# Optimization experiments

Hardware: AMD Instinct MI355X
Metric: run time of the kernel (lower is better)

## Reference

```python
import jax, jax.numpy as jnp
import numpy as np
import math

N, C_IN, H, W = 8, 256, 64, 64
C_ATT, C_OUT = 128, 256
BN_EPS = 1e-5


def conv_bn_relu(x, w, gamma, beta, mean, var):
    # 1x1 conv (no bias) + BatchNorm (eval mode) + ReLU
    y = jnp.einsum('oc,nchw->nohw', w, x)
    inv = gamma / jnp.sqrt(var + BN_EPS)
    y = y * inv[None, :, None, None] + (beta - mean * inv)[None, :, None, None]
    return jax.nn.relu(y)


def setup_inputs() -> dict:
    key = jax.random.key(0)
    ks = jax.random.split(key, 12)
    x = jax.random.normal(ks[0], (N, C_IN, H, W), dtype=jnp.float32)
    mask = jnp.ones((N, 1, H, W), dtype=jnp.float32)
    reduc_w = jax.random.normal(ks[1], (C_OUT, C_IN), dtype=jnp.float32) * (1.0 / math.sqrt(C_IN))
    reduc_gamma = jnp.ones((C_OUT,), dtype=jnp.float32)
    reduc_beta = jnp.zeros((C_OUT,), dtype=jnp.float32)
    reduc_mean = jax.random.normal(ks[2], (C_OUT,), dtype=jnp.float32) * 0.1
    reduc_var = jax.random.uniform(ks[3], (C_OUT,), dtype=jnp.float32) + 0.5
    att_w = jax.random.normal(ks[4], (C_ATT, C_IN), dtype=jnp.float32) * (1.0 / math.sqrt(C_IN))
    att_gamma = jnp.ones((C_ATT,), dtype=jnp.float32)
    att_beta = jnp.zeros((C_ATT,), dtype=jnp.float32)
    att_mean = jax.random.normal(ks[5], (C_ATT,), dtype=jnp.float32) * 0.1
    att_var = jax.random.uniform(ks[6], (C_ATT,), dtype=jnp.float32) + 0.5
    return {
        'x': x, 'mask': mask,
        'reduc_w': reduc_w, 'reduc_gamma': reduc_gamma, 'reduc_beta': reduc_beta,
        'reduc_mean': reduc_mean, 'reduc_var': reduc_var,
        'att_w': att_w, 'att_gamma': att_gamma, 'att_beta': att_beta,
        'att_mean': att_mean, 'att_var': att_var,
    }


def reference(x, mask, reduc_w, reduc_gamma, reduc_beta, reduc_mean, reduc_var,
              att_w, att_gamma, att_beta, att_mean, att_var):
    n, _, h, w = x.shape
    x_feat = conv_bn_relu(x, reduc_w, reduc_gamma, reduc_beta, reduc_mean, reduc_var)   # [n,C_OUT,h,w]
    x_atten = conv_bn_relu(x, att_w, att_gamma, att_beta, att_mean, att_var)            # [n,C_ATT,h,w]
    c = x_atten.shape[1]
    q = x_atten.reshape(n, c, h * w)                                                    # [n,c,HW]
    # energy[n,i,j] = sum_c q[n,c,i]*q[n,c,j] / (1e-8 + sqrt(c))
    energy = jnp.einsum('nci,ncj->nij', q, q) / (1e-8 + math.sqrt(c))
    energy = energy + (mask.reshape(n, 1, h * w) - 1.0) * 1e8
    weight = jax.nn.softmax(energy, axis=2)                                             # [n,HW,HW]
    feat = x_feat.reshape(n, x_feat.shape[1], h * w)                                    # [n,C_OUT,HW]
    out = jnp.einsum('nij,ncj->nci', weight, feat)                                      # [n,C_OUT,HW]
    out = out.reshape(n, feat.shape[1], h, w)
    out = out * mask
    return out
```

## Files before the change

kernel.cpp:

```cpp
#include <hip/hip_runtime.h>
#include <cstdint>
#include <cstddef>

#define NB 8
#define CIN 256
#define HWX 4096
#define CF 256
#define CA 128
#define CT 384

typedef __attribute__((ext_vector_type(8))) _Float16 half8;
typedef __attribute__((ext_vector_type(8))) short short8;
typedef __attribute__((ext_vector_type(4))) short s16x4;
typedef __attribute__((ext_vector_type(4))) float f32x4;
typedef __attribute__((ext_vector_type(4))) unsigned int u32x4;
typedef __attribute__((ext_vector_type(2))) unsigned int u32x2;

#define OFF_WH   0
#define OFF_BIAS (CT*CIN*2)
#define OFF_FEAT (OFF_BIAS + CT*4)
#define OFF_Q    (OFF_FEAT + NB*CF*HWX*2)
#define OFF_NORM (OFF_Q + NB*HWX*CA*2)
#define OFF_G    (OFF_NORM + NB*HWX*4)

__device__ inline unsigned short f16_bits(float f) {
  _Float16 h = (_Float16)f;
  return __builtin_bit_cast(unsigned short, h);
}
__device__ inline half8 ld_half8(const unsigned short* p) {
  short8 r = *(const short8*)p;
  return __builtin_bit_cast(half8, r);
}

__device__ inline void g2l16(const void* g, void* l) {
  __builtin_amdgcn_global_load_lds(
      (const __attribute__((address_space(1))) unsigned int*)g,
      (__attribute__((address_space(3))) unsigned int*)l, 16, 0, 0);
}

__global__ __launch_bounds__(256) void fold_bn_k(
    const float* __restrict__ rw, const float* __restrict__ rg,
    const float* __restrict__ rb, const float* __restrict__ rm, const float* __restrict__ rv,
    const float* __restrict__ aw, const float* __restrict__ ag,
    const float* __restrict__ ab2, const float* __restrict__ am, const float* __restrict__ av,
    unsigned short* __restrict__ wh, float* __restrict__ bias, unsigned* __restrict__ Gmax) {
  int o = blockIdx.x, k = threadIdx.x;
  if (o == 0 && k < NB) Gmax[k] = 0u;
  const float* wsrc; float g, b, m, v;
  if (o < CF) { wsrc = rw + (size_t)o*CIN; g = rg[o]; b = rb[o]; m = rm[o]; v = rv[o]; }
  else { int oa = o - CF; wsrc = aw + (size_t)oa*CIN; g = ag[oa]; b = ab2[oa]; m = am[oa]; v = av[oa]; }
  float inv = g / sqrtf(v + 1e-5f);
  wh[(size_t)o*CIN + k] = f16_bits(wsrc[k] * inv);
  if (k == 0) bias[o] = b - m*inv;
}

__global__ __launch_bounds__(512, 4) void conv_k(
    const float* __restrict__ x, const unsigned short* __restrict__ wh,
    const float* __restrict__ bias, unsigned short* __restrict__ feat,
    unsigned short* __restrict__ q, float* __restrict__ normq,
    unsigned* __restrict__ Gmax) {
  __shared__ unsigned short sX[64*256];
  __shared__ float sGm[4];
  unsigned short (*sQr)[136] = (unsigned short(*)[136])sX;
  int b = blockIdx.x;
  int n = b & 7, pt0 = b >> 3;
  int p0 = pt0 * 64;
  int t = threadIdx.x;
  int w = t >> 6, lane = t & 63, quad = lane >> 4, col = lane & 15;
  const float* xn = x + (size_t)n*CIN*HWX;

  #pragma unroll
  for (int pass=0; pass<4; pass++) {
    int idx = pass*512 + t;
    int kp = idx >> 4, c4 = idx & 15;
    f32x4 a = *(const f32x4*)(xn + (size_t)(2*kp)*HWX + p0 + c4*4);
    f32x4 c = *(const f32x4*)(xn + (size_t)(2*kp+1)*HWX + p0 + c4*4);
    int unit = kp >> 2, off = kp & 3;
    #pragma unroll
    for (int j=0;j<4;j++) {
      int pos = c4*4 + j;
      unsigned dd = (unsigned)f16_bits(a[j]) | ((unsigned)f16_bits(c[j]) << 16);
      *(unsigned*)&sX[pos*256 + ((unit ^ (pos & 31)) << 3) + off*2] = dd;
    }
  }
  __syncthreads();

  f32x4 fzero = {0.f,0.f,0.f,0.f};
  f32x4 acc[4][3];
  #pragma unroll
  for (int pt=0;pt<4;pt++)
    #pragma unroll
    for (int ot=0;ot<3;ot++) acc[pt][ot] = fzero;

  int ocb = w*48;
  half8 B3[3];
  #pragma unroll
  for (int ot=0;ot<3;ot++)
    B3[ot] = ld_half8(wh + (size_t)(ocb + ot*16 + col)*CIN + quad*8);
  #pragma unroll
  for (int ks=0; ks<8; ks++) {
    half8 B3n[3];
    if (ks < 7) {
      #pragma unroll
      for (int ot=0;ot<3;ot++)
        B3n[ot] = ld_half8(wh + (size_t)(ocb + ot*16 + col)*CIN + (ks+1)*32 + quad*8);
    }
    half8 A4[4];
    #pragma unroll
    for (int pt=0;pt<4;pt++) {
      int pos = pt*16 + col;
      A4[pt] = ld_half8(&sX[pos*256 + (((ks*4 + quad) ^ (pos & 31)) << 3)]);
    }
    #pragma unroll
    for (int pt=0;pt<4;pt++)
      #pragma unroll
      for (int ot=0;ot<3;ot++)
        acc[pt][ot] = __builtin_amdgcn_mfma_f32_16x16x32_f16(A4[pt], B3[ot], acc[pt][ot], 0, 0, 0);
    if (ks < 7) {
      #pragma unroll
      for (int ot=0;ot<3;ot++) B3[ot] = B3n[ot];
    }
  }
  __syncthreads();

  float bv[3];
  #pragma unroll
  for (int ot=0;ot<3;ot++) bv[ot] = bias[ocb + ot*16 + col];
  #pragma unroll
  for (int pt=0;pt<4;pt++)
    #pragma unroll
    for (int ot=0;ot<3;ot++) {
      int oc = ocb + ot*16 + col;
      alignas(8) unsigned short u4[4];
      #pragma unroll
      for (int r=0;r<4;r++)
        u4[r] = f16_bits(fmaxf(acc[pt][ot][r] + bv[ot], 0.f));
      if (oc < CF) {
        *(u32x2*)(feat + (size_t)n*CF*HWX + (size_t)oc*HWX + p0 + pt*16 + quad*4) =
            *(const u32x2*)u4;
      } else {
        int cc = oc - CF;
        #pragma unroll
        for (int r=0;r<4;r++)
          sQr[pt*16 + quad*4 + r][cc] = u4[r];
      }
    }
  __syncthreads();

  if (t < 256) {
    int pos = t >> 2, seg = t & 3;
    const unsigned short* src = &sQr[pos][seg*32];
    unsigned short* dst = q + ((size_t)n*HWX + p0 + pos)*CA + seg*32;
    float s2 = 0.f;
    #pragma unroll
    for (int u=0;u<4;u++) {
      short8 v = *(const short8*)(src + u*8);
      *(short8*)(dst + u*8) = v;
      half8 h = __builtin_bit_cast(half8, v);
      #pragma unroll
      for (int e=0;e<8;e++) { float fe = (float)h[e]; s2 += fe*fe; }
    }
    s2 += __shfl_xor(s2, 1, 64);
    s2 += __shfl_xor(s2, 2, 64);
    if (seg == 0) normq[(size_t)n*HWX + p0 + pos] = sqrtf(s2);
    float mx = s2;
    mx = fmaxf(mx, __shfl_xor(mx, 4, 64));
    mx = fmaxf(mx, __shfl_xor(mx, 8, 64));
    mx = fmaxf(mx, __shfl_xor(mx, 16, 64));
    mx = fmaxf(mx, __shfl_xor(mx, 32, 64));
    if (lane == 0) sGm[t >> 6] = sqrtf(mx);
  }
  __syncthreads();
  if (t == 0) {
    float m01 = fmaxf(sGm[0], sGm[1]);
    float m23 = fmaxf(sGm[2], sGm[3]);
    atomicMax(Gmax + n, __float_as_uint(fmaxf(m01, m23)));
  }
}

__global__ __launch_bounds__(512, 4) void flash_k(
    const unsigned short* __restrict__ q, const unsigned short* __restrict__ feat,
    const float* __restrict__ mask, const float* __restrict__ normq,
    const unsigned* __restrict__ Gmax, float* __restrict__ out) {
  __shared__ alignas(16) unsigned short sQ0[64*128];
  __shared__ alignas(16) unsigned short sQ1[64*128];
  __shared__ alignas(16) unsigned short sP0[64][68];
  __shared__ alignas(16) unsigned short sP1[64][68];
  __shared__ float sM0[64];
  __shared__ float sM1[64];
  __shared__ float sL[2][64];
  int b = blockIdx.x;
  int n = b & 7, it = b >> 3;
  int i0 = it * 64;
  int t = threadIdx.x;
  int w = t >> 6, lane = t & 63, quad = lane >> 4, col = lane & 15;
  int wq = w & 3, wh = w >> 2;
  const unsigned short* q_n = q + (size_t)n*HWX*CA;
  const unsigned short* f_n = feat + (size_t)n*CF*HWX;
  const float* m_n = mask + (size_t)n*HWX;
  const int rloc = t >> 4 & 31, oct16 = t & 15;
  const float inv_s = 1.0f/(1e-8f + sqrtf(128.0f));

  auto stage_Q = [&](int j0, unsigned short* sQd, float* sMd) {
    #pragma unroll
    for (int c=0;c<2;c++) {
      int row = c*32 + rloc;
      int og = oct16 ^ (row & 15);
      g2l16(q_n + (size_t)(j0+row)*CA + og*8, &sQd[(size_t)row*128 + oct16*8]);
    }
    if (t < 16) g2l16(m_n + j0 + t*4, &sMd[t*4]);
  };

  half8 ah[4];
  {
    int arow = i0 + wq*16 + col;
    #pragma unroll
    for (int ks=0; ks<4; ks++)
      ah[ks] = ld_half8(q_n + (size_t)arow*CA + ks*32 + quad*8);
  }
  float Gn = __uint_as_float(Gmax[n]);
  float cvals[4];
  #pragma unroll
  for (int r=0;r<4;r++)
    cvals[r] = normq[(size_t)n*HWX + i0 + wq*16 + quad*4 + r] * Gn * inv_s - 5.0f;

  f32x4 fzero = {0.f,0.f,0.f,0.f};
  f32x4 o[4][2];
  #pragma unroll
  for (int ig=0;ig<4;ig++) { o[ig][0] = fzero; o[ig][1] = fzero; }
  float lrun[4] = {0.f,0.f,0.f,0.f};

  auto iter = [&](int ji, unsigned short* sQc, unsigned short (*sPc)[68], float* sMc,
                  unsigned short* sQn, float* sMn) {
    int j0 = ji*64;

    if (ji + 1 < 64) stage_Q(j0+64, sQn, sMn);

    half8 bF[2][2];
    #pragma unroll
    for (int ks2=0;ks2<2;ks2++)
      #pragma unroll
      for (int ct=0;ct<2;ct++) {
        int c = w*32 + ct*16 + col;
        bF[ks2][ct] = ld_half8(f_n + (size_t)c*HWX + j0 + ks2*32 + quad*8);
      }

    f32x4 s[2];
    s[0] = fzero; s[1] = fzero;
    __builtin_amdgcn_s_setprio(1);
    #pragma unroll
    for (int jt=0;jt<2;jt++) {
      int rowj = wh*32 + jt*16 + col;
      #pragma unroll
      for (int ks=0; ks<4; ks++) {
        int slot = (ks*4 + quad) ^ (rowj & 15);
        half8 bq = ld_half8(&sQc[rowj*128 + slot*8]);
        s[jt] = __builtin_amdgcn_mfma_f32_16x16x32_f16(ah[ks], bq, s[jt], 0, 0, 0);
      }
    }
    __builtin_amdgcn_s_setprio(0);

    #pragma unroll
    for (int jt=0;jt<2;jt++) {
      float mj = (sMc[wh*32 + jt*16 + col] - 1.f) * 1e8f;
      #pragma unroll
      for (int r=0;r<4;r++) {
        float pv = __expf(s[jt][r]*inv_s + mj - cvals[r]);
        lrun[r] += pv;
        sPc[wq*16 + quad*4 + r][wh*32 + jt*16 + col] = f16_bits(pv);
      }
    }

    __syncthreads();

    __builtin_amdgcn_s_setprio(1);
    #pragma unroll
    for (int ks2=0; ks2<2; ks2++) {
      half8 aP[4];
      #pragma unroll
      for (int ig=0;ig<4;ig++) {
        const unsigned short* pp = &sPc[ig*16 + col][ks2*32 + quad*8];
        s16x4 lo = *(const s16x4*)pp;
        s16x4 hi = *(const s16x4*)(pp + 4);
        short8 vv = __builtin_shufflevector(lo, hi, 0,1,2,3,4,5,6,7);
        aP[ig] = __builtin_bit_cast(half8, vv);
      }
      #pragma unroll
      for (int ct=0;ct<2;ct++) {
        #pragma unroll
        for (int ig=0;ig<4;ig++)
          o[ig][ct] = __builtin_amdgcn_mfma_f32_16x16x32_f16(aP[ig], bF[ks2][ct], o[ig][ct], 0, 0, 0);
      }
    }
    __builtin_amdgcn_s_setprio(0);
  };

  stage_Q(0, sQ0, sM0);
  __syncthreads();
  #pragma unroll 1
  for (int jj = 0; jj < 32; jj++) {
    iter(2*jj,     sQ0, sP0, sM0, sQ1, sM1);
    iter(2*jj + 1, sQ1, sP1, sM1, sQ0, sM0);
  }

  #pragma unroll
  for (int r=0;r<4;r++) {
    float ss = lrun[r];
    ss += __shfl_xor(ss, 1, 64);
    ss += __shfl_xor(ss, 2, 64);
    ss += __shfl_xor(ss, 4, 64);
    ss += __shfl_xor(ss, 8, 64);
    lrun[r] = ss;
  }
  #pragma unroll
  for (int r=0;r<4;r++)
    if (col == 0) sL[wh][wq*16 + quad*4 + r] = lrun[r];
  __syncthreads();
  #pragma unroll
  for (int ig=0;ig<4;ig++) {
    int base = ig*16 + quad*4;
    f32x4 l0 = *(const f32x4*)&sL[0][base];
    f32x4 l1 = *(const f32x4*)&sL[1][base];
    f32x4 mv = *(const f32x4*)(m_n + i0 + base);
    f32x4 minv;
    #pragma unroll
    for (int r=0;r<4;r++) minv[r] = mv[r] / (l0[r] + l1[r]);
    #pragma unroll
    for (int ct=0;ct<2;ct++) {
      int c = w*32 + ct*16 + col;
      f32x4 v;
      #pragma unroll
      for (int r=0;r<4;r++) v[r] = o[ig][ct][r] * minv[r];
      *(f32x4*)(out + ((size_t)n*CF + c)*HWX + i0 + base) = v;
    }
  }
}

extern "C" void kernel_launch(void* const* d_in, const int* in_sizes, int n_in,
                              void* d_out, int out_size, void* d_ws, size_t ws_size,
                              hipStream_t stream) {
  const float* x    = (const float*)d_in[0];
  const float* mask = (const float*)d_in[1];
  const float* rw   = (const float*)d_in[2];
  const float* rg   = (const float*)d_in[3];
  const float* rb   = (const float*)d_in[4];
  const float* rm   = (const float*)d_in[5];
  const float* rv   = (const float*)d_in[6];
  const float* aw   = (const float*)d_in[7];
  const float* ag   = (const float*)d_in[8];
  const float* ab   = (const float*)d_in[9];
  const float* am   = (const float*)d_in[10];
  const float* av   = (const float*)d_in[11];
  float* out = (float*)d_out;
  char* ws = (char*)d_ws;
  unsigned short* wh = (unsigned short*)(ws + OFF_WH);
  float* bias = (float*)(ws + OFF_BIAS);
  unsigned short* feat = (unsigned short*)(ws + OFF_FEAT);
  unsigned short* q    = (unsigned short*)(ws + OFF_Q);
  float* normq = (float*)(ws + OFF_NORM);
  unsigned* Gmax = (unsigned*)(ws + OFF_G);

  hipLaunchKernelGGL(fold_bn_k, dim3(CT), dim3(CIN), 0, stream,
                     rw, rg, rb, rm, rv, aw, ag, ab, am, av, wh, bias, Gmax);
  hipLaunchKernelGGL(conv_k, dim3(512), dim3(512), 0, stream,
                     x, wh, bias, feat, q, normq, Gmax);
  hipLaunchKernelGGL(flash_k, dim3(512), dim3(512), 0, stream,
                     q, feat, mask, normq, Gmax, out);
}
```

Baseline: 305.3 us.

## Software-pipeline attention loop so PV of previous tile overlaps QK of next

```diff
diff --git a/kernel.cpp b/kernel.cpp
--- a/kernel.cpp
+++ b/kernel.cpp
@@ -230,24 +230,10 @@
   for (int ig=0;ig<4;ig++) { o[ig][0] = fzero; o[ig][1] = fzero; }
   float lrun[4] = {0.f,0.f,0.f,0.f};
 
-  auto iter = [&](int ji, unsigned short* sQc, unsigned short (*sPc)[68], float* sMc,
-                  unsigned short* sQn, float* sMn) {
-    int j0 = ji*64;
-
-    if (ji + 1 < 64) stage_Q(j0+64, sQn, sMn);
-
-    half8 bF[2][2];
-    #pragma unroll
-    for (int ks2=0;ks2<2;ks2++)
-      #pragma unroll
-      for (int ct=0;ct<2;ct++) {
-        int c = w*32 + ct*16 + col;
-        bF[ks2][ct] = ld_half8(f_n + (size_t)c*HWX + j0 + ks2*32 + quad*8);
-      }
-
+  auto qk_sm = [&](const unsigned short* sQc, const float* sMc,
+                   unsigned short (*sPc)[68]) {
     f32x4 s[2];
     s[0] = fzero; s[1] = fzero;
-    __builtin_amdgcn_s_setprio(1);
     #pragma unroll
     for (int jt=0;jt<2;jt++) {
       int rowj = wh*32 + jt*16 + col;
@@ -258,8 +244,6 @@
         s[jt] = __builtin_amdgcn_mfma_f32_16x16x32_f16(ah[ks], bq, s[jt], 0, 0, 0);
       }
     }
-    __builtin_amdgcn_s_setprio(0);
-
     #pragma unroll
     for (int jt=0;jt<2;jt++) {
       float mj = (sMc[wh*32 + jt*16 + col] - 1.f) * 1e8f;
@@ -270,18 +254,24 @@
         sPc[wq*16 + quad*4 + r][wh*32 + jt*16 + col] = f16_bits(pv);
       }
     }
-
-    __syncthreads();
-
-    __builtin_amdgcn_s_setprio(1);
+  };
+  auto pv_f = [&](int j0m, unsigned short (*sPc)[68]) {
+    half8 bF[2][2];
+    #pragma unroll
+    for (int ks2=0;ks2<2;ks2++)
+      #pragma unroll
+      for (int ct=0;ct<2;ct++) {
+        int c = w*32 + ct*16 + col;
+        bF[ks2][ct] = ld_half8(f_n + (size_t)c*HWX + j0m + ks2*32 + quad*8);
+      }
     #pragma unroll
     for (int ks2=0; ks2<2; ks2++) {
       half8 aP[4];
       #pragma unroll
       for (int ig=0;ig<4;ig++) {
-        const unsigned short* pp = &sPc[ig*16 + col][ks2*32 + quad*8];
-        s16x4 lo = *(const s16x4*)pp;
-        s16x4 hi = *(const s16x4*)(pp + 4);
+        const unsigned short* pp2 = &sPc[ig*16 + col][ks2*32 + quad*8];
+        s16x4 lo = *(const s16x4*)pp2;
+        s16x4 hi = *(const s16x4*)(pp2 + 4);
         short8 vv = __builtin_shufflevector(lo, hi, 0,1,2,3,4,5,6,7);
         aP[ig] = __builtin_bit_cast(half8, vv);
       }
@@ -292,16 +282,38 @@
           o[ig][ct] = __builtin_amdgcn_mfma_f32_16x16x32_f16(aP[ig], bF[ks2][ct], o[ig][ct], 0, 0, 0);
       }
     }
+  };
+
+  stage_Q(0, sQ0, sM0);
+  __syncthreads();
+  stage_Q(64, sQ1, sM1);
+  qk_sm(sQ0, sM0, sP0);
+  __syncthreads();
+
+  #pragma unroll 1
+  for (int jj = 0; jj < 31; jj++) {
+    int ji = 2*jj + 1;
+    stage_Q((ji+1)*64, sQ0, sM0);
+    __builtin_amdgcn_s_setprio(1);
+    pv_f((ji-1)*64, sP0);
+    qk_sm(sQ1, sM1, sP1);
     __builtin_amdgcn_s_setprio(0);
-  };
-
-  stage_Q(0, sQ0, sM0);
-  __syncthreads();
-  #pragma unroll 1
-  for (int jj = 0; jj < 32; jj++) {
-    iter(2*jj,     sQ0, sP0, sM0, sQ1, sM1);
-    iter(2*jj + 1, sQ1, sP1, sM1, sQ0, sM0);
-  }
+    __syncthreads();
+    stage_Q((ji+2)*64, sQ1, sM1);
+    __builtin_amdgcn_s_setprio(1);
+    pv_f(ji*64, sP1);
+    qk_sm(sQ0, sM0, sP0);
+    __builtin_amdgcn_s_setprio(0);
+    __syncthreads();
+  }
+
+  __builtin_amdgcn_s_setprio(1);
+  pv_f(62*64, sP0);
+  qk_sm(sQ1, sM1, sP1);
+  __builtin_amdgcn_s_setprio(0);
+  __syncthreads();
+
+  pv_f(63*64, sP1);
 
   #pragma unroll
   for (int r=0;r<4;r++) {
```

New measurement: 322.6 us. 5.7% more time.
